# Performance work log

Hardware: AMD Instinct MI355X
Metric: run time of the kernel (lower is better)

Reference implementation:

```python
import jax, jax.numpy as jnp
import numpy as np

B, S, D, H = 2, 2048, 1024, 16
HD = D // H  # head_dim = 64


def setup_inputs() -> dict:
    key = jax.random.key(0)
    ks = jax.random.split(key, 12)
    xav = (2.0 / (D + D)) ** 0.5  # xavier_normal std for square Linear
    q = jax.random.normal(ks[0], (B, S, D), jnp.float32)
    k = jax.random.normal(ks[1], (B, S, D), jnp.float32)
    v = jax.random.normal(ks[2], (B, S, D), jnp.float32)
    Wq = jax.random.normal(ks[3], (D, D), jnp.float32) * xav
    Wk = jax.random.normal(ks[4], (D, D), jnp.float32) * xav
    Wv = jax.random.normal(ks[5], (D, D), jnp.float32) * xav
    bq = jnp.zeros((D,), jnp.float32)
    bk = jnp.zeros((D,), jnp.float32)
    bv = jnp.zeros((D,), jnp.float32)
    # valid-prefix padding masks (True = valid token); key 0 always valid so
    # no causal softmax row is fully masked (avoids NaN, matches real usage).
    klen = jax.random.randint(ks[6], (B,), S // 2, S + 1)
    qlen = jax.random.randint(ks[7], (B,), S // 2, S + 1)
    pos = jnp.arange(S)
    key_padding_mask = pos[None, :] < klen[:, None]
    query_padding_mask = pos[None, :] < qlen[:, None]
    return {
        "q": q, "k": k, "v": v,
        "Wq": Wq, "bq": bq, "Wk": Wk, "bk": bk, "Wv": Wv, "bv": bv,
        "key_padding_mask": key_padding_mask,
        "query_padding_mask": query_padding_mask,
    }


def _proj_split(x, W, b, n_heads):
    # Linear (y = x W^T + b) then split heads: [B,S,D] -> [B,H,S,hd]
    bsz, sq, dm = x.shape
    hd = dm // n_heads
    y = x @ W.T + b
    return y.reshape(bsz, sq, n_heads, hd).transpose(0, 2, 1, 3)


def reference(q, k, v, Wq, bq, Wk, bk, Wv, bv, key_padding_mask, query_padding_mask):
    bsz, sq, dm = q.shape
    sk = k.shape[1]
    Q = _proj_split(q, Wq, bq, H)  # [B,H,Sq,hd]
    K = _proj_split(k, Wk, bk, H)  # [B,H,Sk,hd]
    V = _proj_split(v, Wv, bv, H)  # [B,H,Sk,hd]
    scale = 1.0 / jnp.sqrt(jnp.asarray(Q.shape[-1], Q.dtype))
    scores = jnp.einsum('bhqd,bhkd->bhqk', Q, K) * scale  # [B,H,Sq,Sk]
    # key padding: -inf where key invalid
    scores = jnp.where(key_padding_mask[:, None, None, :], scores, -jnp.inf)
    # causal: -inf strictly above the diagonal
    causal_ok = jnp.tril(jnp.ones((sq, sk), bool))
    scores = jnp.where(causal_ok[None, None, :, :], scores, -jnp.inf)
    attn = jax.nn.softmax(scores, axis=-1)
    # q_mask: zero out rows for padded queries (post-softmax, as in source)
    attn = jnp.where(query_padding_mask[:, None, :, None], attn, 0.0)
    # dropout p=0.0 -> identity
    out = jnp.einsum('bhqk,bhkd->bhqd', attn, V)
    out = out.transpose(0, 2, 1, 3).reshape(bsz, sq, dm)
    return out + q
```

## Files before the change

### kernel.cpp

```cpp
#include <hip/hip_runtime.h>
#include <stdint.h>

#define BATCH 2
#define SEQ 2048
#define DMODEL 1024
#define NHEAD 16
#define HDIM 64
#define CVT_BLOCKS 15360

typedef __attribute__((ext_vector_type(8))) short bf16x8;
typedef __attribute__((ext_vector_type(4))) float f32x4;

__device__ __forceinline__ unsigned short f2bf(float f) {
  unsigned int u = __float_as_uint(f);
  u += 0x7fffu + ((u >> 16) & 1u);
  return (unsigned short)(u >> 16);
}
__device__ __forceinline__ unsigned int pk2bf(float a, float b) {
  return __builtin_amdgcn_perm(__float_as_uint(b) + 0x8000u,
                               __float_as_uint(a) + 0x8000u, 0x07060302u);
}
__device__ __forceinline__ void async_copy16(const void* g, void* l) {
  __builtin_amdgcn_global_load_lds(
      (const __attribute__((address_space(1))) void*)g,
      (__attribute__((address_space(3))) void*)l, 16, 0, 0);
}

__global__ __launch_bounds__(256) void cvt_all(
    const float* __restrict__ q, const float* __restrict__ k,
    const float* __restrict__ v, const float* __restrict__ Wq,
    const float* __restrict__ Wk, const float* __restrict__ Wv,
    unsigned short* __restrict__ dst,
    const unsigned char* __restrict__ kp, const unsigned char* __restrict__ qp,
    int* __restrict__ lens) {
  if (blockIdx.x == CVT_BLOCKS) {
    const int t = threadIdx.x, wave = t >> 6, lane = t & 63;
    const unsigned char* base = (wave < 2) ? kp : qp;
    const int b = wave & 1;
    const bool bytefmt = (base[1] != 0);
    int cnt = 0;
    if (bytefmt) {
      const uint4* p = (const uint4*)(base + (size_t)b * SEQ);
#pragma unroll
      for (int g = 0; g < 2; g++) {
        const uint4 x = p[g * 64 + lane];
        const unsigned int w[4] = {x.x, x.y, x.z, x.w};
#pragma unroll
        for (int i = 0; i < 4; i++) {
          const unsigned int ww = w[i];
          cnt += ((ww & 0xffu) != 0) + ((ww & 0xff00u) != 0) +
                 ((ww & 0xff0000u) != 0) + ((ww & 0xff000000u) != 0);
        }
      }
    } else {
      const uint4* p = (const uint4*)(base + (size_t)b * SEQ * 4);
#pragma unroll
      for (int g = 0; g < 8; g++) {
        const uint4 x = p[g * 64 + lane];
        cnt += (x.x != 0) + (x.y != 0) + (x.z != 0) + (x.w != 0);
      }
    }
#pragma unroll
    for (int off = 32; off >= 1; off >>= 1) cnt += __shfl_xor(cnt, off, 64);
    if (lane == 0) lens[wave] = cnt;
    return;
  }
  const int g = blockIdx.x * 256 + threadIdx.x;
  const float* src;
  size_t off, dbase;
  if (g < 3 * (1 << 20)) {
    const int ti = g >> 20;
    src = (ti == 0) ? q : (ti == 1) ? k : v;
    off = (size_t)(g & ((1 << 20) - 1));
    dbase = (size_t)ti << 22;
  } else {
    const int gw = g - 3 * (1 << 20);
    const int ti = gw >> 18;
    src = (ti == 0) ? Wq : (ti == 1) ? Wk : Wv;
    off = (size_t)(gw & ((1 << 18) - 1));
    dbase = (3ull << 22) + ((size_t)ti << 20);
  }
  const float4 x = ((const float4*)src)[off];
  ushort4 o;
  o.x = f2bf(x.x); o.y = f2bf(x.y); o.z = f2bf(x.z); o.w = f2bf(x.w);
  *(ushort4*)(dst + dbase + off * 4) = o;
}

__global__ __launch_bounds__(256) void qkv_proj(
    const unsigned short* __restrict__ xq, const unsigned short* __restrict__ xk,
    const unsigned short* __restrict__ xv,
    const unsigned short* __restrict__ Wq, const float* __restrict__ bq,
    const unsigned short* __restrict__ Wk, const float* __restrict__ bk,
    const unsigned short* __restrict__ Wv, const float* __restrict__ bv,
    unsigned short* __restrict__ Qo, unsigned short* __restrict__ Ko,
    unsigned short* __restrict__ Vo, const int* __restrict__ lens) {
  const int z = blockIdx.z;
  const int m0 = blockIdx.y * 128, n0 = blockIdx.x * 128;
  const int b = m0 >> 11;
  const int len = (z == 0) ? lens[2 + b] : lens[b];
  if ((m0 & (SEQ - 1)) >= len) return;

  const unsigned short* x = (z == 0) ? xq : (z == 1) ? xk : xv;
  const unsigned short* W = (z == 0) ? Wq : (z == 1) ? Wk : Wv;
  const float* bias = (z == 0) ? bq : (z == 1) ? bk : bv;
  unsigned short* dst = (z == 0) ? Qo : (z == 1) ? Ko : Vo;
  const float osc = (z == 0) ? 0.18033688011112042f : 1.0f;

  __shared__ unsigned short As[128 * 64];
  __shared__ unsigned short Bs[128 * 64];

  const int t = threadIdx.x;
  const int wave = t >> 6, lane = t & 63, quad = lane >> 4, l16 = lane & 15;
  const int wm = wave >> 1, wn = wave & 1;

  const f32x4 fz = {0.f, 0.f, 0.f, 0.f};
  f32x4 acc[4][4];
#pragma unroll
  for (int i = 0; i < 4; i++)
#pragma unroll
    for (int j = 0; j < 4; j++) acc[i][j] = fz;

  for (int k0 = 0; k0 < DMODEL; k0 += 64) {
    __syncthreads();
#pragma unroll
    for (int c = 0; c < 4; c++) {
      const int slot = c * 256 + t;
      const int row = slot >> 3, pg = slot & 7;
      const int lg = (pg ^ (row & 7)) * 8;
      async_copy16(x + (size_t)(m0 + row) * DMODEL + k0 + lg,
                   (char*)As + (c * 256 + (t & 192)) * 16);
      async_copy16(W + (size_t)(n0 + row) * DMODEL + k0 + lg,
                   (char*)Bs + (c * 256 + (t & 192)) * 16);
    }
    __syncthreads();
#pragma unroll
    for (int kk = 0; kk < 2; kk++) {
      bf16x8 af[4], bfr[4];
#pragma unroll
      for (int i = 0; i < 4; i++) {
        const int ra = wm * 64 + i * 16 + l16;
        const int rb = wn * 64 + i * 16 + l16;
        af[i] = *(const bf16x8*)(As + ra * 64 + ((kk * 4 + quad) ^ (ra & 7)) * 8);
        bfr[i] = *(const bf16x8*)(Bs + rb * 64 + ((kk * 4 + quad) ^ (rb & 7)) * 8);
      }
      if (z == 2) {
#pragma unroll
        for (int i = 0; i < 4; i++)
#pragma unroll
          for (int j = 0; j < 4; j++)
            acc[i][j] = __builtin_amdgcn_mfma_f32_16x16x32_bf16(af[i], bfr[j], acc[i][j], 0, 0, 0);
      } else {
#pragma unroll
        for (int i = 0; i < 4; i++)
#pragma unroll
          for (int j = 0; j < 4; j++)
            acc[i][j] = __builtin_amdgcn_mfma_f32_16x16x32_bf16(bfr[j], af[i], acc[i][j], 0, 0, 0);
      }
    }
  }

  if (z == 2) {
#pragma unroll
    for (int j = 0; j < 4; j++) {
      const int n = n0 + wn * 64 + j * 16 + l16;
      const float bb_ = bias[n];
      const int h = n >> 6, hd = n & 63;
#pragma unroll
      for (int i = 0; i < 4; i++) {
        const int s0 = (m0 & (SEQ - 1)) + wm * 64 + i * 16 + quad * 4;
        uint2 w;
        w.x = pk2bf(acc[i][j][0] + bb_, acc[i][j][1] + bb_);
        w.y = pk2bf(acc[i][j][2] + bb_, acc[i][j][3] + bb_);
        *(uint2*)(dst + (((size_t)(b * NHEAD + h) * HDIM + hd) << 11) + s0) = w;
      }
    }
  } else {
#pragma unroll
    for (int j = 0; j < 4; j++) {
      const int nb = n0 + wn * 64 + j * 16 + quad * 4;
      const float4 b4 = *(const float4*)(bias + nb);
      const int h = nb >> 6, hd0 = nb & 63;
#pragma unroll
      for (int i = 0; i < 4; i++) {
        const int s = (m0 & (SEQ - 1)) + wm * 64 + i * 16 + l16;
        uint2 w;
        w.x = pk2bf((acc[i][j][0] + b4.x) * osc, (acc[i][j][1] + b4.y) * osc);
        w.y = pk2bf((acc[i][j][2] + b4.z) * osc, (acc[i][j][3] + b4.w) * osc);
        *(uint2*)(dst + (((size_t)(b * NHEAD + h) * SEQ + s) << 6) + hd0) = w;
      }
    }
  }
}


#define KVB 64

template <bool MASKED>
__device__ __forceinline__ void softmax_update(
    const f32x4 s[4], int key0, int qrow, int klen, int quad, int l16,
    float& mst, float& lsum, f32x4 o[4], unsigned short* Pdst) {
  float pm[4][4];
  float rm = -__builtin_inff();
  if (MASKED) {
    const int kmax = ((qrow < klen - 1) ? qrow : klen - 1) - key0 - quad * 4;
#pragma unroll
    for (int nf = 0; nf < 4; nf++)
#pragma unroll
      for (int r = 0; r < 4; r++) {
        pm[nf][r] = (nf * 16 + r <= kmax) ? s[nf][r] : -__builtin_inff();
        rm = fmaxf(rm, pm[nf][r]);
      }
  } else {
#pragma unroll
    for (int nf = 0; nf < 4; nf++)
#pragma unroll
      for (int r = 0; r < 4; r++) {
        pm[nf][r] = s[nf][r];
        rm = fmaxf(rm, pm[nf][r]);
      }
  }
  rm = fmaxf(rm, __shfl_xor(rm, 16, 64));
  rm = fmaxf(rm, __shfl_xor(rm, 32, 64));
  if (__ballot(rm > mst) != 0ull) {
    const float mnew = fmaxf(mst, rm);
    const float alpha = exp2f(fmaxf(mst, -1e30f) - fmaxf(mnew, -1e30f));
    mst = mnew;
    lsum *= alpha;
    float ab[4];
#pragma unroll
    for (int r = 0; r < 4; r++) ab[r] = __shfl(alpha, quad * 4 + r, 64);
#pragma unroll
    for (int db = 0; db < 4; db++)
#pragma unroll
      for (int r = 0; r < 4; r++) o[db][r] *= ab[r];
  }
  const float mref = fmaxf(mst, -1e30f);
  float rs = 0.f;
#pragma unroll
  for (int nf = 0; nf < 4; nf++)
#pragma unroll
    for (int r = 0; r < 4; r++) {
      const float p = exp2f(pm[nf][r] - mref);
      pm[nf][r] = p;
      rs += p;
    }
  rs += __shfl_xor(rs, 16, 64);
  rs += __shfl_xor(rs, 32, 64);
  lsum += rs;
#pragma unroll
  for (int nf = 0; nf < 4; nf++) {
    uint2 w;
    w.x = pk2bf(pm[nf][0], pm[nf][1]);
    w.y = pk2bf(pm[nf][2], pm[nf][3]);
    const int g = (nf * 2 + (quad >> 1)) ^ (l16 & 7);
    *(uint2*)(Pdst + l16 * KVB + g * 8 + (quad & 1) * 4) = w;
  }
}

template <bool MASKED>
__device__ __forceinline__ void tile_pass(
    const unsigned short* __restrict__ ks, const unsigned short* __restrict__ vt,
    unsigned short* __restrict__ Pw, bf16x8 qf0, bf16x8 qf1,
    int key0, int qrow, int klen, int quad, int l16,
    float& mst, float& lsum, f32x4 o[4]) {
  const f32x4 fz = {0.f, 0.f, 0.f, 0.f};
  f32x4 s[4];
  __builtin_amdgcn_s_setprio(1);
#pragma unroll
  for (int nf = 0; nf < 4; nf++) {
    const int row = nf * 16 + l16;
    const int sw = row & 7;
    const bf16x8 kf0 = *(const bf16x8*)(ks + row * 64 + (quad ^ sw) * 8);
    const bf16x8 kf1 = *(const bf16x8*)(ks + row * 64 + ((quad + 4) ^ sw) * 8);
    f32x4 a = fz;
    a = __builtin_amdgcn_mfma_f32_16x16x32_bf16(kf0, qf0, a, 0, 0, 0);
    a = __builtin_amdgcn_mfma_f32_16x16x32_bf16(kf1, qf1, a, 0, 0, 0);
    s[nf] = a;
  }
  __builtin_amdgcn_s_setprio(0);
  softmax_update<MASKED>(s, key0, qrow, klen, quad, l16, mst, lsum, o, Pw);
  bf16x8 pf[2];
#pragma unroll
  for (int ksn = 0; ksn < 2; ksn++)
    pf[ksn] = *(const bf16x8*)(Pw + l16 * KVB + ((ksn * 4 + quad) ^ (l16 & 7)) * 8);
  __builtin_amdgcn_s_setprio(1);
#pragma unroll
  for (int db = 0; db < 4; db++) {
    const int d = db * 16 + l16;
    const int sw = d & 7;
#pragma unroll
    for (int ksn = 0; ksn < 2; ksn++) {
      const bf16x8 v = *(const bf16x8*)(vt + d * KVB + ((ksn * 4 + quad) ^ sw) * 8);
      o[db] = __builtin_amdgcn_mfma_f32_16x16x32_bf16(pf[ksn], v, o[db], 0, 0, 0);
    }
  }
  __builtin_amdgcn_s_setprio(0);
}

__global__ __launch_bounds__(512, 2) void attn_kernel(
    const unsigned short* __restrict__ Qb, const unsigned short* __restrict__ Kb,
    const unsigned short* __restrict__ VTb, const float* __restrict__ qin,
    const int* __restrict__ lens, float* __restrict__ out) {
  const int pi = blockIdx.x, h = blockIdx.y, b = blockIdx.z;
  const int bh = b * NHEAD + h;
  const int t = threadIdx.x, wave = t >> 6, lane = t & 63, quad = lane >> 4, l16 = lane & 15;
  const int grp = wave >> 2, w4 = wave & 3;
  const int lo = pi, hi = 31 - pi;
  const int myTile = grp ? hi : lo;
  const int klen = lens[b], qlen = lens[2 + b];

  __shared__ unsigned short Ks[2][KVB * 64];
  __shared__ unsigned short VT[2][KVB * 64];
  __shared__ unsigned short Ps[8][16 * KVB];

  const unsigned short* Qp = Qb + (size_t)bh * SEQ * HDIM;
  const unsigned short* Kp = Kb + (size_t)bh * SEQ * HDIM;
  const unsigned short* Vt = VTb + (size_t)bh * HDIM * SEQ;

  const int qrow = myTile * 64 + w4 * 16 + l16;
  const bf16x8 qf0 = *(const bf16x8*)(Qp + (size_t)qrow * HDIM + quad * 8);
  const bf16x8 qf1 = *(const bf16x8*)(Qp + (size_t)qrow * HDIM + 32 + quad * 8);

  const f32x4 fz = {0.f, 0.f, 0.f, 0.f};
  f32x4 o[4];
#pragma unroll
  for (int i = 0; i < 4; i++) o[i] = fz;
  float mst = -__builtin_inff(), lsum = 0.f;

  const int ktLO = lo + 1;
  int ktHI = 0;
  if (hi * 64 < qlen) {
    const int kendHI = ((hi * 64 + 64) < klen) ? (hi * 64 + 64) : klen;
    ktHI = (kendHI + 63) >> 6;
  }
  const int ktot = (ktLO > ktHI) ? ktLO : ktHI;
  const int myt = grp ? ktHI : ktLO;

  auto STAGE = [&](int buf, int kt) {
    const int key0 = kt << 6;
    const int row = t >> 3;
    const int sg = ((t & 7) ^ (row & 7)) * 8;
    async_copy16(Kp + (size_t)(key0 + row) * HDIM + sg,
                 (char*)Ks[buf] + (t & 448) * 16);
    async_copy16(Vt + (size_t)row * SEQ + key0 + sg,
                 (char*)VT[buf] + (t & 448) * 16);
  };

  STAGE(0, 0);
  __syncthreads();
  int cur = 0;
  for (int kt = 0; kt < ktot; kt++) {
    if (kt + 1 < ktot) STAGE(cur ^ 1, kt + 1);
    if (kt < myt) {
      const int key0 = kt << 6;
      if ((key0 + 63 <= myTile * 64 + w4 * 16) && (key0 + 63 < klen))
        tile_pass<false>(Ks[cur], VT[cur], Ps[wave], qf0, qf1, key0, qrow,
                         klen, quad, l16, mst, lsum, o);
      else
        tile_pass<true>(Ks[cur], VT[cur], Ps[wave], qf0, qf1, key0, qrow,
                        klen, quad, l16, mst, lsum, o);
    }
    __syncthreads();
    cur ^= 1;
  }

  const float inv = (lsum > 0.f) ? 1.f / lsum : 0.f;
  float ib[4];
#pragma unroll
  for (int r = 0; r < 4; r++) ib[r] = __shfl(inv, quad * 4 + r, 64);
#pragma unroll
  for (int db = 0; db < 4; db++) {
    const int col = h * HDIM + db * 16 + l16;
#pragma unroll
    for (int r = 0; r < 4; r++) {
      const int i = myTile * 64 + w4 * 16 + quad * 4 + r;
      const size_t oo = (size_t)(b * SEQ + i) * DMODEL + col;
      out[oo] = ((i < qlen) ? o[db][r] * ib[r] : 0.f) + qin[oo];
    }
  }
}

extern "C" void kernel_launch(void* const* d_in, const int* in_sizes, int n_in,
                              void* d_out, int out_size, void* d_ws, size_t ws_size,
                              hipStream_t stream) {
  (void)in_sizes; (void)n_in; (void)out_size; (void)ws_size;
  const float* q = (const float*)d_in[0];
  const float* k = (const float*)d_in[1];
  const float* v = (const float*)d_in[2];
  const float* Wq = (const float*)d_in[3];
  const float* bq = (const float*)d_in[4];
  const float* Wk = (const float*)d_in[5];
  const float* bk = (const float*)d_in[6];
  const float* Wv = (const float*)d_in[7];
  const float* bv = (const float*)d_in[8];
  const unsigned char* kpm = (const unsigned char*)d_in[9];
  const unsigned char* qpm = (const unsigned char*)d_in[10];
  float* out = (float*)d_out;

  const size_t tsz = (size_t)BATCH * SEQ * DMODEL;
  const size_t wsz = (size_t)DMODEL * DMODEL;

  char* ws = (char*)d_ws;
  int* lens = (int*)ws;
  unsigned short* cvt_base = (unsigned short*)(ws + 256);
  unsigned short* qb16 = cvt_base;
  unsigned short* kb16 = qb16 + tsz;
  unsigned short* vb16 = kb16 + tsz;
  unsigned short* Wqb = vb16 + tsz;
  unsigned short* Wkb = Wqb + wsz;
  unsigned short* Wvb = Wkb + wsz;
  unsigned short* Qw = Wvb + wsz;
  unsigned short* Kw = Qw + tsz;
  unsigned short* Vtw = Kw + tsz;

  cvt_all<<<dim3(CVT_BLOCKS + 1), dim3(256), 0, stream>>>(q, k, v, Wq, Wk, Wv,
                                                          cvt_base, kpm, qpm, lens);
  qkv_proj<<<dim3(8, 32, 3), dim3(256), 0, stream>>>(qb16, kb16, vb16, Wqb, bq, Wkb, bk, Wvb, bv, Qw, Kw, Vtw, lens);
  attn_kernel<<<dim3(16, NHEAD, BATCH), dim3(512), 0, stream>>>(Qw, Kw, Vtw, q, lens, out);
}
```

Baseline: 206.1 us.

## Split paired causal tiles into separate 4-wave blocks and lazy-rescale softmax

Each attention block used to pair a low and a high query tile, with 8 waves sharing the K/V stages. It now handles a single 64-row query tile with 4 waves, launches twice as many blocks, and skips all K/V staging for tiles that fall past the query length. The online-softmax rescale is also deferred until the running max grows by more than 8, which cuts the exp and multiply work on O. In exchange, K/V loads are no longer shared between the paired tiles, causal load balance now depends on block scheduling, and deferred rescaling risks exponent overflow headroom.

New measurement: 217.4 us. 1.06x slower.

```diff
diff --git a/kernel.cpp b/kernel.cpp
--- a/kernel.cpp
+++ b/kernel.cpp
@@ -221,7 +221,7 @@
   }
   rm = fmaxf(rm, __shfl_xor(rm, 16, 64));
   rm = fmaxf(rm, __shfl_xor(rm, 32, 64));
-  if (__ballot(rm > mst) != 0ull) {
+  if (__ballot(rm > mst + 8.0f) != 0ull) {
     const float mnew = fmaxf(mst, rm);
     const float alpha = exp2f(fmaxf(mst, -1e30f) - fmaxf(mnew, -1e30f));
     mst = mnew;
@@ -297,27 +297,24 @@
   __builtin_amdgcn_s_setprio(0);
 }
 
-__global__ __launch_bounds__(512, 2) void attn_kernel(
+__global__ __launch_bounds__(256, 4) void attn_kernel(
     const unsigned short* __restrict__ Qb, const unsigned short* __restrict__ Kb,
     const unsigned short* __restrict__ VTb, const float* __restrict__ qin,
     const int* __restrict__ lens, float* __restrict__ out) {
-  const int pi = blockIdx.x, h = blockIdx.y, b = blockIdx.z;
+  const int tile = blockIdx.x, h = blockIdx.y, b = blockIdx.z;
   const int bh = b * NHEAD + h;
   const int t = threadIdx.x, wave = t >> 6, lane = t & 63, quad = lane >> 4, l16 = lane & 15;
-  const int grp = wave >> 2, w4 = wave & 3;
-  const int lo = pi, hi = 31 - pi;
-  const int myTile = grp ? hi : lo;
   const int klen = lens[b], qlen = lens[2 + b];
 
   __shared__ unsigned short Ks[2][KVB * 64];
   __shared__ unsigned short VT[2][KVB * 64];
-  __shared__ unsigned short Ps[8][16 * KVB];
+  __shared__ unsigned short Ps[4][16 * KVB];
 
   const unsigned short* Qp = Qb + (size_t)bh * SEQ * HDIM;
   const unsigned short* Kp = Kb + (size_t)bh * SEQ * HDIM;
   const unsigned short* Vt = VTb + (size_t)bh * HDIM * SEQ;
 
-  const int qrow = myTile * 64 + w4 * 16 + l16;
+  const int qrow = tile * 64 + wave * 16 + l16;
   const bf16x8 qf0 = *(const bf16x8*)(Qp + (size_t)qrow * HDIM + quad * 8);
   const bf16x8 qf1 = *(const bf16x8*)(Qp + (size_t)qrow * HDIM + 32 + quad * 8);
 
@@ -327,41 +324,42 @@
   for (int i = 0; i < 4; i++) o[i] = fz;
   float mst = -__builtin_inff(), lsum = 0.f;
 
-  const int ktLO = lo + 1;
-  int ktHI = 0;
-  if (hi * 64 < qlen) {
-    const int kendHI = ((hi * 64 + 64) < klen) ? (hi * 64 + 64) : klen;
-    ktHI = (kendHI + 63) >> 6;
-  }
-  const int ktot = (ktLO > ktHI) ? ktLO : ktHI;
-  const int myt = grp ? ktHI : ktLO;
+  int ktot = 0;
+  if (tile * 64 < qlen) {
+    const int kend = ((tile * 64 + 64) < klen) ? (tile * 64 + 64) : klen;
+    ktot = (kend + 63) >> 6;
+  }
 
   auto STAGE = [&](int buf, int kt) {
     const int key0 = kt << 6;
-    const int row = t >> 3;
-    const int sg = ((t & 7) ^ (row & 7)) * 8;
-    async_copy16(Kp + (size_t)(key0 + row) * HDIM + sg,
-                 (char*)Ks[buf] + (t & 448) * 16);
-    async_copy16(Vt + (size_t)row * SEQ + key0 + sg,
-                 (char*)VT[buf] + (t & 448) * 16);
+#pragma unroll
+    for (int u = 0; u < 2; u++) {
+      const int c = u * 256 + t;
+      const int row = c >> 3;
+      const int sg = ((t & 7) ^ (row & 7)) * 8;
+      async_copy16(Kp + (size_t)(key0 + row) * HDIM + sg,
+                   (char*)Ks[buf] + (u * 256 + (t & 192)) * 16);
+      async_copy16(Vt + (size_t)row * SEQ + key0 + sg,
+                   (char*)VT[buf] + (u * 256 + (t & 192)) * 16);
+    }
   };
 
-  STAGE(0, 0);
-  __syncthreads();
-  int cur = 0;
-  for (int kt = 0; kt < ktot; kt++) {
-    if (kt + 1 < ktot) STAGE(cur ^ 1, kt + 1);
-    if (kt < myt) {
+  if (ktot > 0) {
+    STAGE(0, 0);
+    __syncthreads();
+    int cur = 0;
+    for (int kt = 0; kt < ktot; kt++) {
+      if (kt + 1 < ktot) STAGE(cur ^ 1, kt + 1);
       const int key0 = kt << 6;
-      if ((key0 + 63 <= myTile * 64 + w4 * 16) && (key0 + 63 < klen))
+      if ((key0 + 63 <= tile * 64 + wave * 16) && (key0 + 63 < klen))
         tile_pass<false>(Ks[cur], VT[cur], Ps[wave], qf0, qf1, key0, qrow,
                          klen, quad, l16, mst, lsum, o);
       else
         tile_pass<true>(Ks[cur], VT[cur], Ps[wave], qf0, qf1, key0, qrow,
                         klen, quad, l16, mst, lsum, o);
-    }
-    __syncthreads();
-    cur ^= 1;
+      __syncthreads();
+      cur ^= 1;
+    }
   }
 
   const float inv = (lsum > 0.f) ? 1.f / lsum : 0.f;
@@ -373,7 +371,7 @@
     const int col = h * HDIM + db * 16 + l16;
 #pragma unroll
     for (int r = 0; r < 4; r++) {
-      const int i = myTile * 64 + w4 * 16 + quad * 4 + r;
+      const int i = tile * 64 + wave * 16 + quad * 4 + r;
       const size_t oo = (size_t)(b * SEQ + i) * DMODEL + col;
       out[oo] = ((i < qlen) ? o[db][r] * ib[r] : 0.f) + qin[oo];
     }
@@ -416,5 +414,5 @@
   cvt_all<<<dim3(CVT_BLOCKS + 1), dim3(256), 0, stream>>>(q, k, v, Wq, Wk, Wv,
                                                           cvt_base, kpm, qpm, lens);
   qkv_proj<<<dim3(8, 32, 3), dim3(256), 0, stream>>>(qb16, kb16, vb16, Wqb, bq, Wkb, bk, Wvb, bv, Qw, Kw, Vtw, lens);
-  attn_kernel<<<dim3(16, NHEAD, BATCH), dim3(512), 0, stream>>>(Qw, Kw, Vtw, q, lens, out);
-}
+  attn_kernel<<<dim3(32, NHEAD, BATCH), dim3(256), 0, stream>>>(Qw, Kw, Vtw, q, lens, out);
+}
```
